# Performance work log

Hardware: AMD Instinct MI355X
Metric: run time of the kernel (lower is better)

The kernel has to match this reference:

```python
import jax, jax.numpy as jnp
import numpy as np

N = 100000   # nodes
E = 1600000  # edges (avg degree 16)
D = 128      # input feature dim
H = 128      # hidden_channels
O = 64       # out_channels


def _uniform(key, shape, fan_in):
    bound = 1.0 / np.sqrt(fan_in)
    return jax.random.uniform(key, shape, jnp.float32, -bound, bound)


def setup_inputs() -> dict:
    key = jax.random.key(0)
    ks = jax.random.split(key, 9)
    x = jax.random.normal(ks[0], (N, D), jnp.float32)
    edge_index = jax.random.randint(ks[1], (2, E), 0, N, dtype=jnp.int32)
    return {
        "x": x,
        "edge_index": edge_index,
        # layer 1: SAGEConv(D -> H): lin_l (on aggregated neighbors, with bias), lin_r (root)
        "W1l": _uniform(ks[2], (D, H), D),
        "b1": _uniform(ks[3], (H,), D),
        "W1r": _uniform(ks[4], (D, H), D),
        # layer 2: SAGEConv(H -> O)
        "W2l": _uniform(ks[5], (H, O), H),
        "b2": _uniform(ks[6], (O,), H),
        "W2r": _uniform(ks[7], (H, O), H),
    }


def sage_conv(x, edge_index, Wl, b, Wr):
    """PyG SAGEConv with mean aggregation: lin_l(mean_{j in N(i)} x_j) + lin_r(x_i)."""
    src, dst = edge_index[0], edge_index[1]
    n = x.shape[0]
    msg = x[src]                                                 # [E, D] gather
    agg = jax.ops.segment_sum(msg, dst, num_segments=n)         # [N, D] scatter-add
    cnt = jax.ops.segment_sum(jnp.ones((src.shape[0],), x.dtype), dst, num_segments=n)
    agg = agg / jnp.maximum(cnt, 1.0)[:, None]                  # mean; isolated nodes -> 0
    return agg @ Wl + b + x @ Wr


def reference(x, edge_index, W1l, b1, W1r, W2l, b2, W2r):
    h = jax.nn.relu(sage_conv(x, edge_index, W1l, b1, W1r))
    return sage_conv(h, edge_index, W2l, b2, W2r)
```

## Files before the change

kernel.cpp:

```cpp
#include <hip/hip_runtime.h>
#include <stdint.h>

#define NN 100000
#define NE 1600000
#define MAXDEG 64
#define NSLICE 8
#define SLICE_SZ 12500
#define CHUNK 6400

typedef __attribute__((ext_vector_type(8))) short short8;
typedef __attribute__((ext_vector_type(4))) float f32x4;

__device__ __forceinline__ float bflo(unsigned v) { return __uint_as_float(v << 16); }
__device__ __forceinline__ float bfhi(unsigned v) { return __uint_as_float(v & 0xffff0000u); }
__device__ __forceinline__ unsigned short f2bf(float f) {
  unsigned u = __float_as_uint(f);
  u += 0x7fff + ((u >> 16) & 1);
  return (unsigned short)(u >> 16);
}

__global__ __launch_bounds__(256) void build_buckets(const int* __restrict__ src,
                                                     const int* __restrict__ dst,
                                                     int* __restrict__ cnt,
                                                     int* __restrict__ buck) {
  const int slice = blockIdx.x & (NSLICE - 1);
  const int chunk = blockIdx.x >> 3;
  const int c0 = chunk * CHUNK;
  const int lo = slice * SLICE_SZ, hi = lo + SLICE_SZ;
  for (int e = c0 + (int)threadIdx.x * 4; e < c0 + CHUNK; e += 1024) {
    int4 d = *(const int4*)(dst + e);
    int4 s = *(const int4*)(src + e);
    if (d.x >= lo && d.x < hi) { int p = atomicAdd(&cnt[d.x], 1); if (p < MAXDEG) buck[d.x * MAXDEG + p] = s.x; }
    if (d.y >= lo && d.y < hi) { int p = atomicAdd(&cnt[d.y], 1); if (p < MAXDEG) buck[d.y * MAXDEG + p] = s.y; }
    if (d.z >= lo && d.z < hi) { int p = atomicAdd(&cnt[d.z], 1); if (p < MAXDEG) buck[d.z * MAXDEG + p] = s.z; }
    if (d.w >= lo && d.w < hi) { int p = atomicAdd(&cnt[d.w], 1); if (p < MAXDEG) buck[d.w * MAXDEG + p] = s.w; }
  }
}

__global__ __launch_bounds__(256) void to_bf16(const float* __restrict__ x,
                                               unsigned* __restrict__ xb) {
  int i = blockIdx.x * 256 + threadIdx.x;
  if (i >= NN * 32) return;
  float4 v = ((const float4*)x)[i];
  uint2 o;
  o.x = ((unsigned)f2bf(v.y) << 16) | f2bf(v.x);
  o.y = ((unsigned)f2bf(v.w) << 16) | f2bf(v.z);
  ((uint2*)xb)[i] = o;
}

__global__ __launch_bounds__(256) void transpose_w(const float* __restrict__ W1l,
                                                   const float* __restrict__ W1r,
                                                   const float* __restrict__ W2l,
                                                   const float* __restrict__ W2r,
                                                   unsigned short* __restrict__ WT1,
                                                   unsigned short* __restrict__ WT2) {
  int t = blockIdx.x * 256 + threadIdx.x;
  if (t < 128 * 256) {
    int m = t >> 8, k = t & 255;
    float v = (k < 128) ? W1l[k * 128 + m] : W1r[(k - 128) * 128 + m];
    WT1[t] = f2bf(v);
  } else {
    int i = t - 128 * 256;
    if (i < 64 * 256) {
      int m = i >> 8, k = i & 255;
      float v = (k < 128) ? W2l[k * 64 + m] : W2r[(k - 128) * 64 + m];
      WT2[i] = f2bf(v);
    }
  }
}

__global__ __launch_bounds__(256) void aggregate(const unsigned* __restrict__ xb,
                                                 const int* __restrict__ cnt,
                                                 const int* __restrict__ buck,
                                                 unsigned* __restrict__ agg) {
  int wid = (blockIdx.x * 256 + threadIdx.x) >> 6;
  int lane = threadIdx.x & 63;
  if (wid >= NN) return;
  int deg = cnt[wid];
  int dcl = min(deg, MAXDEG);
  int slot = buck[(size_t)wid * MAXDEG + lane];
  float a0 = 0.f, a1 = 0.f;
  if (dcl > 0) {
    int last = dcl - 1;
    for (int p = 0; p < dcl; p += 16) {
      unsigned v[16];
#pragma unroll
      for (int j = 0; j < 16; j++) {
        int s = __shfl(slot, min(p + j, last), 64);
        v[j] = xb[(size_t)s * 64 + lane];
      }
#pragma unroll
      for (int j = 0; j < 16; j++) {
        unsigned vj = (p + j <= last) ? v[j] : 0u;
        a0 += bflo(vj); a1 += bfhi(vj);
      }
    }
  }
  float inv = 1.f / (float)max(deg, 1);
  a0 *= inv; a1 *= inv;
  agg[(size_t)wid * 64 + lane] = ((unsigned)f2bf(a1) << 16) | f2bf(a0);
}

template <int M, bool RELU, typename OutT>
__global__ __launch_bounds__(256) void sage_gemm(const unsigned* __restrict__ agg,
                                                 const unsigned* __restrict__ xb,
                                                 const unsigned short* __restrict__ WT,
                                                 const float* __restrict__ bias,
                                                 OutT* __restrict__ out) {
  constexpr int LDA = 264;
  __shared__ unsigned short sA[64][LDA];

  const int t = threadIdx.x;
  const int node0 = blockIdx.x * 64;

  for (int i = t; i < 64 * 32; i += 256) {
    int row = i >> 5, c = i & 31;
    int node = node0 + row;
    uint4 v = {0u, 0u, 0u, 0u};
    if (node < NN)
      v = (c < 16) ? ((const uint4*)(agg + (size_t)node * 64))[c]
                   : ((const uint4*)(xb + (size_t)node * 64))[c - 16];
    *(uint4*)&sA[row][c * 8] = v;
  }
  __syncthreads();

  const int lane = t & 63;
  const int wv = t >> 6;
  const int m = lane & 15;
  const int q = lane >> 4;

  f32x4 acc[M / 16];
#pragma unroll
  for (int c = 0; c < M / 16; c++) acc[c] = {0.f, 0.f, 0.f, 0.f};

#pragma unroll
  for (int ks = 0; ks < 8; ks++) {
    short8 a = *(const short8*)&sA[wv * 16 + m][ks * 32 + q * 8];
#pragma unroll
    for (int c = 0; c < M / 16; c++) {
      short8 b = *(const short8*)(WT + (size_t)(c * 16 + m) * 256 + ks * 32 + q * 8);
      acc[c] = __builtin_amdgcn_mfma_f32_16x16x32_bf16(a, b, acc[c], 0, 0, 0);
    }
  }

#pragma unroll
  for (int c = 0; c < M / 16; c++) {
    int col = c * 16 + m;
    float bc = bias[col];
#pragma unroll
    for (int r = 0; r < 4; r++) {
      int lr = wv * 16 + q * 4 + r;
      float v = acc[c][r] + bc;
      if (RELU) v = fmaxf(v, 0.f);
      if constexpr (sizeof(OutT) == 2) sA[lr][col] = f2bf(v);
      else ((float*)&sA[lr][0])[col] = v;
    }
  }
#pragma unroll
  for (int it = 0; it < 4; it++) {
    int idx = it * 64 + lane;
    int rr = idx >> 4, cc = idx & 15;
    int node = node0 + wv * 16 + rr;
    if (node < NN) {
      uint4 v = *(const uint4*)((const char*)&sA[wv * 16 + rr][0] + cc * 16);
      *(uint4*)((char*)(out + (size_t)node * M) + cc * 16) = v;
    }
  }
}

extern "C" void kernel_launch(void* const* d_in, const int* in_sizes, int n_in,
                              void* d_out, int out_size, void* d_ws, size_t ws_size,
                              hipStream_t stream) {
  const float* x   = (const float*)d_in[0];
  const int*   ei  = (const int*)d_in[1];
  const float* W1l = (const float*)d_in[2];
  const float* b1  = (const float*)d_in[3];
  const float* W1r = (const float*)d_in[4];
  const float* W2l = (const float*)d_in[5];
  const float* b2  = (const float*)d_in[6];
  const float* W2r = (const float*)d_in[7];
  float* out = (float*)d_out;

  char* ws = (char*)d_ws;
  int* cnt  = (int*)ws;                                   ws += (512 << 10);
  int* buck = (int*)ws;                                   ws += (size_t)NN * MAXDEG * 4;
  unsigned* xbf = (unsigned*)ws;                          ws += (size_t)NN * 64 * 4;
  unsigned* aggb = (unsigned*)ws;                         ws += (size_t)NN * 64 * 4;
  unsigned* hb = (unsigned*)ws;                           ws += (size_t)NN * 64 * 4;
  unsigned short* WT1 = (unsigned short*)ws;              ws += 128 * 256 * 2;
  unsigned short* WT2 = (unsigned short*)ws;              ws += 64 * 256 * 2;

  const int* src = ei;
  const int* dst = ei + NE;

  hipMemsetAsync(cnt, 0, (size_t)NN * 4, stream);
  build_buckets<<<NSLICE * (NE / CHUNK), 256, 0, stream>>>(src, dst, cnt, buck);
  to_bf16<<<(NN * 32 + 255) / 256, 256, 0, stream>>>(x, xbf);
  transpose_w<<<192, 256, 0, stream>>>(W1l, W1r, W2l, W2r, WT1, WT2);

  aggregate<<<(NN * 64 + 255) / 256, 256, 0, stream>>>(xbf, cnt, buck, aggb);
  sage_gemm<128, true, unsigned short><<<(NN + 63) / 64, 256, 0, stream>>>(
      aggb, xbf, WT1, b1, (unsigned short*)hb);

  aggregate<<<(NN * 64 + 255) / 256, 256, 0, stream>>>(hb, cnt, buck, aggb);
  sage_gemm<64, false, float><<<(NN + 63) / 64, 256, 0, stream>>>(
      aggb, hb, WT2, b2, out);
}
```

Before: 398.2 us.

## Fuse neighbor mean aggregation into the SAGE GEMM kernel

Removes the separate aggregate kernel. Each wave of the GEMM kernel now gathers and averages the neighbor features for its own 16 nodes and writes them, with the root features, straight into shared memory before the MFMA step. This drops the intermediate aggregated-feature buffer (a full write and read per layer) and two kernel launches. The cost is much less parallelism during the gather: each wave now handles 16 nodes one after another instead of one node per wave, and it holds large register arrays. That can weaken latency hiding for the random gathers.

```diff
diff --git a/kernel.cpp b/kernel.cpp
--- a/kernel.cpp
+++ b/kernel.cpp
@@ -69,63 +69,59 @@
   }
 }
 
-__global__ __launch_bounds__(256) void aggregate(const unsigned* __restrict__ xb,
-                                                 const int* __restrict__ cnt,
-                                                 const int* __restrict__ buck,
-                                                 unsigned* __restrict__ agg) {
-  int wid = (blockIdx.x * 256 + threadIdx.x) >> 6;
-  int lane = threadIdx.x & 63;
-  if (wid >= NN) return;
-  int deg = cnt[wid];
-  int dcl = min(deg, MAXDEG);
-  int slot = buck[(size_t)wid * MAXDEG + lane];
-  float a0 = 0.f, a1 = 0.f;
-  if (dcl > 0) {
-    int last = dcl - 1;
-    for (int p = 0; p < dcl; p += 16) {
-      unsigned v[16];
-#pragma unroll
-      for (int j = 0; j < 16; j++) {
-        int s = __shfl(slot, min(p + j, last), 64);
-        v[j] = xb[(size_t)s * 64 + lane];
-      }
-#pragma unroll
-      for (int j = 0; j < 16; j++) {
-        unsigned vj = (p + j <= last) ? v[j] : 0u;
-        a0 += bflo(vj); a1 += bfhi(vj);
-      }
-    }
-  }
-  float inv = 1.f / (float)max(deg, 1);
-  a0 *= inv; a1 *= inv;
-  agg[(size_t)wid * 64 + lane] = ((unsigned)f2bf(a1) << 16) | f2bf(a0);
-}
-
 template <int M, bool RELU, typename OutT>
-__global__ __launch_bounds__(256) void sage_gemm(const unsigned* __restrict__ agg,
-                                                 const unsigned* __restrict__ xb,
-                                                 const unsigned short* __restrict__ WT,
-                                                 const float* __restrict__ bias,
-                                                 OutT* __restrict__ out) {
+__global__ __launch_bounds__(256) void sage_fused(const unsigned* __restrict__ xb,
+                                                  const int* __restrict__ cnt,
+                                                  const int* __restrict__ buck,
+                                                  const unsigned short* __restrict__ WT,
+                                                  const float* __restrict__ bias,
+                                                  OutT* __restrict__ out) {
   constexpr int LDA = 264;
   __shared__ unsigned short sA[64][LDA];
 
   const int t = threadIdx.x;
-  const int node0 = blockIdx.x * 64;
-
-  for (int i = t; i < 64 * 32; i += 256) {
-    int row = i >> 5, c = i & 31;
-    int node = node0 + row;
-    uint4 v = {0u, 0u, 0u, 0u};
-    if (node < NN)
-      v = (c < 16) ? ((const uint4*)(agg + (size_t)node * 64))[c]
-                   : ((const uint4*)(xb + (size_t)node * 64))[c - 16];
-    *(uint4*)&sA[row][c * 8] = v;
-  }
-  __syncthreads();
-
   const int lane = t & 63;
   const int wv = t >> 6;
+  const int node0 = blockIdx.x * 64;
+  const int nb = node0 + wv * 16;
+
+  int slot[16]; unsigned xr[16]; int deg[16];
+#pragma unroll
+  for (int i = 0; i < 16; i++) {
+    int node = nb + i;
+    if (node < NN) {
+      slot[i] = buck[(size_t)node * MAXDEG + lane];
+      xr[i]   = xb[(size_t)node * 64 + lane];
+      deg[i]  = cnt[node];
+    } else { slot[i] = 0; xr[i] = 0u; deg[i] = 0; }
+  }
+
+#pragma unroll
+  for (int i = 0; i < 16; i++) {
+    float a0 = 0.f, a1 = 0.f;
+    int dcl = min(deg[i], MAXDEG);
+    if (dcl > 0) {
+      int last = dcl - 1;
+      for (int p = 0; p < dcl; p += 16) {
+        unsigned v[16];
+#pragma unroll
+        for (int j = 0; j < 16; j++) {
+          int s = __shfl(slot[i], min(p + j, last), 64);
+          v[j] = xb[(size_t)s * 64 + lane];
+        }
+#pragma unroll
+        for (int j = 0; j < 16; j++) {
+          unsigned vj = (p + j <= last) ? v[j] : 0u;
+          a0 += bflo(vj); a1 += bfhi(vj);
+        }
+      }
+    }
+    float inv = 1.f / (float)max(deg[i], 1);
+    unsigned pk = ((unsigned)f2bf(a1 * inv) << 16) | f2bf(a0 * inv);
+    ((unsigned*)&sA[wv * 16 + i][0])[lane]   = pk;
+    ((unsigned*)&sA[wv * 16 + i][128])[lane] = xr[i];
+  }
+
   const int m = lane & 15;
   const int q = lane >> 4;
 
@@ -185,7 +181,6 @@
   int* cnt  = (int*)ws;                                   ws += (512 << 10);
   int* buck = (int*)ws;                                   ws += (size_t)NN * MAXDEG * 4;
   unsigned* xbf = (unsigned*)ws;                          ws += (size_t)NN * 64 * 4;
-  unsigned* aggb = (unsigned*)ws;                         ws += (size_t)NN * 64 * 4;
   unsigned* hb = (unsigned*)ws;                           ws += (size_t)NN * 64 * 4;
   unsigned short* WT1 = (unsigned short*)ws;              ws += 128 * 256 * 2;
   unsigned short* WT2 = (unsigned short*)ws;              ws += 64 * 256 * 2;
@@ -198,11 +193,9 @@
   to_bf16<<<(NN * 32 + 255) / 256, 256, 0, stream>>>(x, xbf);
   transpose_w<<<192, 256, 0, stream>>>(W1l, W1r, W2l, W2r, WT1, WT2);
 
-  aggregate<<<(NN * 64 + 255) / 256, 256, 0, stream>>>(xbf, cnt, buck, aggb);
-  sage_gemm<128, true, unsigned short><<<(NN + 63) / 64, 256, 0, stream>>>(
-      aggb, xbf, WT1, b1, (unsigned short*)hb);
-
-  aggregate<<<(NN * 64 + 255) / 256, 256, 0, stream>>>(hb, cnt, buck, aggb);
-  sage_gemm<64, false, float><<<(NN + 63) / 64, 256, 0, stream>>>(
-      aggb, hb, WT2, b2, out);
-}
+  sage_fused<128, true, unsigned short><<<(NN + 63) / 64, 256, 0, stream>>>(
+      xbf, cnt, buck, WT1, b1, (unsigned short*)hb);
+
+  sage_fused<64, false, float><<<(NN + 63) / 64, 256, 0, stream>>>(
+      hb, cnt, buck, WT2, b2, out);
+}
```

Result: faster. 378.3 us (-5.0%).
